# Kernel optimization log

Hardware: AMD Instinct MI355X
Metric: run time of the kernel (lower is better)

## Reference

```python
import jax, jax.numpy as jnp
import numpy as np

N_NODES = 20000
N_EDGES = 320000
F_IN = 128
H = 4        # heads per layer
D = 128      # per-head hidden dim
NEG_SLOPE = 0.2


def setup_inputs() -> dict:
    key = jax.random.key(0)
    ks = jax.random.split(key, 14)
    s = 0.05
    inp = {
        "feats": jax.random.normal(ks[0], (N_NODES, F_IN), jnp.float32),
        "src": jax.random.randint(ks[1], (N_EDGES,), 0, N_NODES, jnp.int64),
        "dst": jax.random.randint(ks[2], (N_EDGES,), 0, N_NODES, jnp.int64),
        # layer 1: in F_IN -> H heads x D, flatten agg
        "W1": s * jax.random.normal(ks[3], (F_IN, H * D), jnp.float32),
        "al1": s * jax.random.normal(ks[4], (H, D), jnp.float32),
        "ar1": s * jax.random.normal(ks[5], (H, D), jnp.float32),
        "b1": jnp.zeros((H * D,), jnp.float32),
        # layer 2: in H*D -> H heads x D, mean agg
        "W2": s * jax.random.normal(ks[6], (H * D, H * D), jnp.float32),
        "al2": s * jax.random.normal(ks[7], (H, D), jnp.float32),
        "ar2": s * jax.random.normal(ks[8], (H, D), jnp.float32),
        "b2": jnp.zeros((H * D,), jnp.float32),
        # readout Linear(D, 1)
        "Wr": s * jax.random.normal(ks[9], (D, 1), jnp.float32),
        "br": jnp.zeros((1,), jnp.float32),
    }
    return inp


def _gat_conv(x, src, dst, W, al, ar, b, n_nodes):
    """dgl GATConv: per-head linear, edge softmax over incoming edges, scatter-sum."""
    h, d = al.shape
    z = (x @ W).reshape(n_nodes, h, d)                      # [N,H,D]
    el = jnp.einsum('nhd,hd->nh', z, al)                    # [N,H]
    er = jnp.einsum('nhd,hd->nh', z, ar)                    # [N,H]
    e = jax.nn.leaky_relu(el[src] + er[dst], NEG_SLOPE)     # [E,H]
    # numerically stable softmax grouped by destination node
    emax = jax.lax.stop_gradient(jax.ops.segment_max(e, dst, num_segments=n_nodes))
    a = jnp.exp(e - emax[dst])                              # [E,H]
    denom = jax.ops.segment_sum(a, dst, num_segments=n_nodes)
    alpha = a / jnp.maximum(denom[dst], 1e-9)               # [E,H]
    out = jax.ops.segment_sum(alpha[:, :, None] * z[src], dst, num_segments=n_nodes)
    return out + b.reshape(1, h, d)                         # [N,H,D]


def reference(feats, src, dst, W1, al1, ar1, b1, W2, al2, ar2, b2, Wr, br):
    n = feats.shape[0]
    h1 = _gat_conv(feats, src, dst, W1, al1, ar1, b1, n)    # [N,H,D]
    h1 = jax.nn.elu(h1.reshape(n, -1))                      # flatten heads -> [N,H*D]
    h2 = _gat_conv(h1, src, dst, W2, al2, ar2, b2, n)       # [N,H,D]
    h2 = h2.mean(axis=1)                                    # mean over heads -> [N,D]
    node_preds = h2 @ Wr + br                               # [N,1]
    return node_preds.sum(axis=0)                           # [1]
```

## Files before the change

### kernel.cpp

```cpp
#include <hip/hip_runtime.h>
#include <hip/hip_bf16.h>
#include <cstddef>

constexpr int NN = 20000;
constexpr int NE = 320000;
constexpr int NHEAD = 4;
constexpr int ND = 128;
constexpr int HD = 512;
constexpr int MPAD = 20096;
constexpr int SLOTS = 64;
constexpr float NEG_SLOPE = 0.2f;

using short8 = __attribute__((ext_vector_type(8))) short;
using f32x4 = __attribute__((ext_vector_type(4))) float;
using f32x2 = __attribute__((ext_vector_type(2))) float;

__device__ inline void gload16(const void* g, void* l) {
  __builtin_amdgcn_global_load_lds(
      (const __attribute__((address_space(1))) void*)g,
      (__attribute__((address_space(3))) void*)l, 16, 0, 0);
}

__device__ inline unsigned char f32_to_fp8(float v) {
  int pk = __builtin_amdgcn_cvt_pk_fp8_f32(v, v, 0, false);
  return (unsigned char)(pk & 0xff);
}

__global__ __launch_bounds__(256) void fill_kernel(const int* __restrict__ dst,
                                                   const int* __restrict__ src,
                                                   int* __restrict__ cnt,
                                                   int* __restrict__ src_perm) {
  int t = blockIdx.x * 256 + threadIdx.x;
  if (t < NE) {
    int d = dst[t];
    int p = atomicAdd(&cnt[d], 1);
    if (p < SLOTS) src_perm[d * SLOTS + p] = src[t];
  }
}

constexpr int P0 = MPAD * 128;
constexpr int P1 = P0 + 512 * 128;
constexpr int P2 = P1 + 512 * 512;
constexpr int P3 = P2 + (MPAD - NN) * HD;
constexpr int P4 = P3 + 256;
__global__ __launch_bounds__(256) void prep_kernel(
    const float* __restrict__ feats, const float* __restrict__ W1,
    const float* __restrict__ W2,
    __hip_bfloat16* __restrict__ featsb, __hip_bfloat16* __restrict__ W1t,
    __hip_bfloat16* __restrict__ W2t, __hip_bfloat16* __restrict__ hb,
    float* __restrict__ partials) {
  int t = blockIdx.x * 256 + threadIdx.x;
  if (t < P0) {
    featsb[t] = __float2bfloat16(t < NN * 128 ? feats[t] : 0.f);
  } else if (t < P1) {
    int u = t - P0;
    W1t[u] = __float2bfloat16(W1[(size_t)(u & 127) * 512 + (u >> 7)]);
  } else if (t < P2) {
    int u = t - P1;
    W2t[u] = __float2bfloat16(W2[(size_t)(u & 511) * 512 + (u >> 9)]);
  } else if (t < P3) {
    int u = t - P2;
    hb[(size_t)NN * HD + u] = __float2bfloat16(0.f);
  } else if (t < P4) {
    partials[t - P3] = 0.f;
  }
}

__global__ __launch_bounds__(256) void mfma_gemm_kernel(
    const __hip_bfloat16* __restrict__ A,
    const __hip_bfloat16* __restrict__ Bt,
    unsigned char* __restrict__ Cout,
    int K,
    const float* __restrict__ al,
    const float* __restrict__ ar,
    const float* __restrict__ wq,
    float* __restrict__ el,
    float* __restrict__ er,
    float* __restrict__ q) {
  __shared__ short As[128 * 32];
  __shared__ short Bs[128 * 32];
  __shared__ float elbuf[4][128];
  __shared__ float erbuf[4][128];
  __shared__ float qbuf[4][128];
  int t = threadIdx.x;
  int lane = t & 63;
  int wave = t >> 6;
  int rowBase = blockIdx.x * 128;
  int head = blockIdx.y;
  int colBase = head * 128;
  int woffr = (wave & 1) * 64;
  int woffc = (wave >> 1) * 64;
  int mrow = lane & 15, quad = lane >> 4;

  f32x4 acc[4][4];
#pragma unroll
  for (int i = 0; i < 4; ++i)
#pragma unroll
    for (int j = 0; j < 4; ++j) acc[i][j] = (f32x4){0.f, 0.f, 0.f, 0.f};

  for (int k0 = 0; k0 < K; k0 += 32) {
#pragma unroll
    for (int p = 0; p < 2; ++p) {
      int f = p * 256 + wave * 64 + lane;
      int r = f >> 2, kc = f & 3;
      gload16(A + (size_t)(rowBase + r) * K + k0 + kc * 8,
              As + p * 2048 + wave * 512);
      gload16(Bt + (size_t)(colBase + r) * K + k0 + kc * 8,
              Bs + p * 2048 + wave * 512);
    }
    __syncthreads();
    short8 af[4], bfr[4];
#pragma unroll
    for (int i = 0; i < 4; ++i)
      af[i] = *(const short8*)&As[(woffr + i * 16 + mrow) * 32 + quad * 8];
#pragma unroll
    for (int j = 0; j < 4; ++j)
      bfr[j] = *(const short8*)&Bs[(woffc + j * 16 + mrow) * 32 + quad * 8];
#pragma unroll
    for (int i = 0; i < 4; ++i)
#pragma unroll
      for (int j = 0; j < 4; ++j)
        acc[i][j] = __builtin_amdgcn_mfma_f32_16x16x32_bf16(af[i], bfr[j], acc[i][j], 0, 0, 0);
    __syncthreads();
  }

  if (Cout) {
#pragma unroll
    for (int i = 0; i < 4; ++i) {
#pragma unroll
      for (int j = 0; j < 4; ++j) {
        int col = colBase + woffc + j * 16 + mrow;
#pragma unroll
        for (int r = 0; r < 4; ++r) {
          int row = rowBase + woffr + i * 16 + quad * 4 + r;
          Cout[(size_t)row * HD + col] = f32_to_fp8(acc[i][j][r]);
        }
      }
    }
  }

  float al_v[4], ar_v[4], wq_v[4];
#pragma unroll
  for (int j = 0; j < 4; ++j) {
    int coll = woffc + j * 16 + mrow;
    al_v[j] = al[head * 128 + coll];
    ar_v[j] = ar[head * 128 + coll];
    wq_v[j] = wq ? wq[coll] : 0.f;
  }
#pragma unroll
  for (int i = 0; i < 4; ++i) {
#pragma unroll
    for (int r = 0; r < 4; ++r) {
      float pl = 0.f, pr = 0.f, pq = 0.f;
#pragma unroll
      for (int j = 0; j < 4; ++j) {
        float v = acc[i][j][r];
        pl += v * al_v[j];
        pr += v * ar_v[j];
        pq += v * wq_v[j];
      }
#pragma unroll
      for (int off = 1; off < 16; off <<= 1) {
        pl += __shfl_xor(pl, off);
        pr += __shfl_xor(pr, off);
        pq += __shfl_xor(pq, off);
      }
      if (mrow == 0) {
        int row128 = woffr + i * 16 + quad * 4 + r;
        elbuf[wave][row128] = pl;
        erbuf[wave][row128] = pr;
        qbuf[wave][row128] = pq;
      }
    }
  }
  __syncthreads();
  if (t < 128) {
    int row = t;
    int w0 = (row < 64) ? 0 : 1;
    float ev = elbuf[w0][row] + elbuf[w0 + 2][row];
    float rv = erbuf[w0][row] + erbuf[w0 + 2][row];
    float qv = qbuf[w0][row] + qbuf[w0 + 2][row];
    int gr = rowBase + row;
    if (gr < NN) {
      el[gr * 4 + head] = ev;
      er[gr * 4 + head] = rv;
      if (wq) q[gr * 4 + head] = qv;
    }
  }
}

__global__ __launch_bounds__(256) void aggregate_kernel(
    const unsigned char* __restrict__ zf8,
    const int* __restrict__ cnt,
    const int* __restrict__ src_perm,
    const float* __restrict__ el,
    const float* __restrict__ er,
    const float* __restrict__ bias,
    __hip_bfloat16* __restrict__ out) {
  __shared__ float4 alds[4][SLOTS];
  int wv = __builtin_amdgcn_readfirstlane((int)(threadIdx.x >> 6));
  int n = blockIdx.x * 4 + wv;
  int lane = threadIdx.x & 63;
  int c = min(cnt[n], SLOTS);
  int base = n * SLOTS;

  {
    float4 er4 = *reinterpret_cast<const float4*>(&er[n * 4]);
    float a0 = 0.f, a1 = 0.f, a2 = 0.f, a3 = 0.f;
    if (lane < c) {
      int s = src_perm[base + lane];
      float4 e4 = *reinterpret_cast<const float4*>(&el[s * 4]);
      float x0 = e4.x + er4.x, x1 = e4.y + er4.y;
      float x2 = e4.z + er4.z, x3 = e4.w + er4.w;
      x0 = (x0 > 0.f) ? x0 : NEG_SLOPE * x0;
      x1 = (x1 > 0.f) ? x1 : NEG_SLOPE * x1;
      x2 = (x2 > 0.f) ? x2 : NEG_SLOPE * x2;
      x3 = (x3 > 0.f) ? x3 : NEG_SLOPE * x3;
      a0 = __expf(x0); a1 = __expf(x1); a2 = __expf(x2); a3 = __expf(x3);
    }
    float s0 = a0, s1 = a1, s2 = a2, s3 = a3;
#pragma unroll
    for (int off = 1; off < 64; off <<= 1) {
      s0 += __shfl_xor(s0, off);
      s1 += __shfl_xor(s1, off);
      s2 += __shfl_xor(s2, off);
      s3 += __shfl_xor(s3, off);
    }
    float4 av;
    av.x = a0 / fmaxf(s0, 1e-9f);
    av.y = a1 / fmaxf(s1, 1e-9f);
    av.z = a2 / fmaxf(s2, 1e-9f);
    av.w = a3 / fmaxf(s3, 1e-9f);
    alds[wv][lane] = av;
  }

  int head = lane >> 4;
  float acc[8] = {};

#define EDGE_BODY(IDX)                                                         \
  {                                                                            \
    int s = src_perm[base + (IDX)];                                            \
    float4 a4 = alds[wv][(IDX)];                                               \
    float a = (head & 2) ? ((head & 1) ? a4.w : a4.z)                          \
                         : ((head & 1) ? a4.y : a4.x);                         \
    uint2 w = *reinterpret_cast<const uint2*>(zf8 + (size_t)s * 512 + lane * 8); \
    f32x2 f0 = __builtin_amdgcn_cvt_pk_f32_fp8(w.x, false);                    \
    f32x2 f1 = __builtin_amdgcn_cvt_pk_f32_fp8(w.x, true);                     \
    f32x2 f2 = __builtin_amdgcn_cvt_pk_f32_fp8(w.y, false);                    \
    f32x2 f3 = __builtin_amdgcn_cvt_pk_f32_fp8(w.y, true);                     \
    acc[0] += a * f0.x; acc[1] += a * f0.y;                                    \
    acc[2] += a * f1.x; acc[3] += a * f1.y;                                    \
    acc[4] += a * f2.x; acc[5] += a * f2.y;                                    \
    acc[6] += a * f3.x; acc[7] += a * f3.y;                                    \
  }

  int i = 0;
  for (; i + 3 < c; i += 4) {
    EDGE_BODY(i)
    EDGE_BODY(i + 1)
    EDGE_BODY(i + 2)
    EDGE_BODY(i + 3)
  }
  for (; i < c; ++i) EDGE_BODY(i)
#undef EDGE_BODY

  float4 bA = *reinterpret_cast<const float4*>(&bias[lane * 8]);
  float4 bB = *reinterpret_cast<const float4*>(&bias[lane * 8 + 4]);
  float v[8];
  v[0] = acc[0] + bA.x; v[1] = acc[1] + bA.y;
  v[2] = acc[2] + bA.z; v[3] = acc[3] + bA.w;
  v[4] = acc[4] + bB.x; v[5] = acc[5] + bB.y;
  v[6] = acc[6] + bB.z; v[7] = acc[7] + bB.w;
#pragma unroll
  for (int j = 0; j < 8; ++j) v[j] = (v[j] > 0.f) ? v[j] : expm1f(v[j]);
  __hip_bfloat162 o[4];
#pragma unroll
  for (int j = 0; j < 4; ++j)
    o[j] = __float22bfloat162_rn(make_float2(v[2 * j], v[2 * j + 1]));
  *reinterpret_cast<uint4*>(out + (size_t)n * HD + lane * 8) =
      *reinterpret_cast<const uint4*>(o);
}

__global__ __launch_bounds__(256) void attn_q_kernel(
    const int* __restrict__ src_perm,
    const int* __restrict__ cnt,
    const float* __restrict__ el,
    const float* __restrict__ er,
    const float* __restrict__ q,
    float* __restrict__ partials) {
  __shared__ float blk[4];
  int wv = __builtin_amdgcn_readfirstlane((int)(threadIdx.x >> 6));
  int n = blockIdx.x * 4 + wv;
  int lane = threadIdx.x & 63;
  int c = min(cnt[n], SLOTS);
  float4 er4 = *reinterpret_cast<const float4*>(&er[n * 4]);
  float a0 = 0.f, a1 = 0.f, a2 = 0.f, a3 = 0.f;
  int s = 0;
  if (lane < c) {
    s = src_perm[n * SLOTS + lane];
    float4 e4 = *reinterpret_cast<const float4*>(&el[s * 4]);
    float x0 = e4.x + er4.x, x1 = e4.y + er4.y;
    float x2 = e4.z + er4.z, x3 = e4.w + er4.w;
    x0 = (x0 > 0.f) ? x0 : NEG_SLOPE * x0;
    x1 = (x1 > 0.f) ? x1 : NEG_SLOPE * x1;
    x2 = (x2 > 0.f) ? x2 : NEG_SLOPE * x2;
    x3 = (x3 > 0.f) ? x3 : NEG_SLOPE * x3;
    a0 = __expf(x0); a1 = __expf(x1); a2 = __expf(x2); a3 = __expf(x3);
  }
  float s0 = a0, s1 = a1, s2 = a2, s3 = a3;
#pragma unroll
  for (int off = 1; off < 64; off <<= 1) {
    s0 += __shfl_xor(s0, off);
    s1 += __shfl_xor(s1, off);
    s2 += __shfl_xor(s2, off);
    s3 += __shfl_xor(s3, off);
  }
  float p = 0.f;
  if (lane < c) {
    float4 q4 = *reinterpret_cast<const float4*>(&q[s * 4]);
    p = (a0 / fmaxf(s0, 1e-9f)) * q4.x + (a1 / fmaxf(s1, 1e-9f)) * q4.y +
        (a2 / fmaxf(s2, 1e-9f)) * q4.z + (a3 / fmaxf(s3, 1e-9f)) * q4.w;
  }
#pragma unroll
  for (int off = 32; off > 0; off >>= 1) p += __shfl_down(p, off);
  if (lane == 0) blk[wv] = p;
  __syncthreads();
  if (threadIdx.x == 0) {
    atomicAdd(&partials[blockIdx.x & 255], blk[0] + blk[1] + blk[2] + blk[3]);
  }
}

__global__ __launch_bounds__(512) void final_kernel(
    const float* __restrict__ partials, const float* __restrict__ b2,
    const float* __restrict__ Wr, const float* __restrict__ br,
    float* __restrict__ out) {
  __shared__ float tmp[512];
  int t = threadIdx.x;
  float sum = (t < 256) ? partials[t] : 0.f;
  sum += (float)NN * b2[t] * Wr[t & 127];
  tmp[t] = sum;
  __syncthreads();
  for (int off = 256; off > 0; off >>= 1) {
    if (t < off) tmp[t] += tmp[t + off];
    __syncthreads();
  }
  if (t == 0) out[0] = 0.25f * tmp[0] + (float)NN * br[0];
}

extern "C" void kernel_launch(void* const* d_in, const int* in_sizes, int n_in,
                              void* d_out, int out_size, void* d_ws, size_t ws_size,
                              hipStream_t stream) {
  const float* feats = (const float*)d_in[0];
  const int* src = (const int*)d_in[1];
  const int* dst = (const int*)d_in[2];
  const float* W1 = (const float*)d_in[3];
  const float* al1 = (const float*)d_in[4];
  const float* ar1 = (const float*)d_in[5];
  const float* b1 = (const float*)d_in[6];
  const float* W2 = (const float*)d_in[7];
  const float* al2 = (const float*)d_in[8];
  const float* ar2 = (const float*)d_in[9];
  const float* b2 = (const float*)d_in[10];
  const float* Wr = (const float*)d_in[11];
  const float* br = (const float*)d_in[12];
  float* out = (float*)d_out;

  __hip_bfloat16* featsb = (__hip_bfloat16*)d_ws;
  unsigned char* zf8 = (unsigned char*)(featsb + (size_t)MPAD * 128);
  __hip_bfloat16* hb = (__hip_bfloat16*)(zf8 + (size_t)MPAD * HD);
  __hip_bfloat16* W1t = hb + (size_t)MPAD * HD;
  __hip_bfloat16* W2t = W1t + 512 * 128;
  float* el = (float*)(W2t + 512 * 512);
  float* er = el + (size_t)NN * NHEAD;
  float* qv = er + (size_t)NN * NHEAD;
  float* partials = qv + (size_t)NN * NHEAD;
  int* cnt = (int*)(partials + 256);
  int* src_perm = cnt + NN;

  hipMemsetAsync(cnt, 0, NN * sizeof(int), stream);
  fill_kernel<<<(NE + 255) / 256, 256, 0, stream>>>(dst, src, cnt, src_perm);

  prep_kernel<<<(P4 + 255) / 256, 256, 0, stream>>>(feats, W1, W2, featsb, W1t,
                                                    W2t, hb, partials);

  dim3 gemm_grid(MPAD / 128, NHEAD);

  mfma_gemm_kernel<<<gemm_grid, 256, 0, stream>>>(featsb, W1t, zf8, 128,
                                                  al1, ar1, nullptr, el, er, nullptr);
  aggregate_kernel<<<NN / 4, 256, 0, stream>>>(zf8, cnt, src_perm, el, er, b1, hb);

  mfma_gemm_kernel<<<gemm_grid, 256, 0, stream>>>(hb, W2t, nullptr, 512,
                                                  al2, ar2, Wr, el, er, qv);
  attn_q_kernel<<<NN / 4, 256, 0, stream>>>(src_perm, cnt, el, er, qv, partials);
  final_kernel<<<1, 512, 0, stream>>>(partials, b2, Wr, br, out);
}
```

Measured before the change: 193.7 us.

## Fold layer-2 GEMM into precomputed projection vectors fused into aggregation

Layer 2 only needs el2, er2 and the readout projection q per node and head. So W2 is pre-multiplied with al2, ar2 and Wr into 12 combined 512-length vectors. The aggregation kernel then dots each ELU output row with these vectors directly. This removes the second 20000x512x512 MFMA GEMM, the bf16 h1 buffer write and the W2 transpose. It also merges fill into prep and folds the final reduction into attn_q through a last-block atomic counter, which drops two launches. The cost is extra per-wave shuffle reductions in aggregate and a serial 128-long dot per thread in prep.

```diff
diff --git a/kernel.cpp b/kernel.cpp
--- a/kernel.cpp
+++ b/kernel.cpp
@@ -26,62 +26,60 @@
   return (unsigned char)(pk & 0xff);
 }
 
-__global__ __launch_bounds__(256) void fill_kernel(const int* __restrict__ dst,
-                                                   const int* __restrict__ src,
-                                                   int* __restrict__ cnt,
-                                                   int* __restrict__ src_perm) {
+constexpr int S0 = NE;
+constexpr int S1 = S0 + MPAD * 128;
+constexpr int S2 = S1 + 512 * 128;
+constexpr int S3 = S2 + 12 * 512;
+constexpr int S4 = S3 + 256;
+constexpr int S5 = S4 + 16;
+__global__ __launch_bounds__(256) void prep_kernel(
+    const float* __restrict__ feats, const float* __restrict__ W1,
+    const float* __restrict__ W2, const float* __restrict__ al2,
+    const float* __restrict__ ar2, const float* __restrict__ Wr,
+    const int* __restrict__ src, const int* __restrict__ dst,
+    __hip_bfloat16* __restrict__ featsb, __hip_bfloat16* __restrict__ W1t,
+    float* __restrict__ vcomb, float* __restrict__ partials,
+    unsigned int* __restrict__ done,
+    int* __restrict__ cnt, int* __restrict__ src_perm) {
   int t = blockIdx.x * 256 + threadIdx.x;
-  if (t < NE) {
+  if (t < S0) {
     int d = dst[t];
     int p = atomicAdd(&cnt[d], 1);
     if (p < SLOTS) src_perm[d * SLOTS + p] = src[t];
-  }
-}
-
-constexpr int P0 = MPAD * 128;
-constexpr int P1 = P0 + 512 * 128;
-constexpr int P2 = P1 + 512 * 512;
-constexpr int P3 = P2 + (MPAD - NN) * HD;
-constexpr int P4 = P3 + 256;
-__global__ __launch_bounds__(256) void prep_kernel(
-    const float* __restrict__ feats, const float* __restrict__ W1,
-    const float* __restrict__ W2,
-    __hip_bfloat16* __restrict__ featsb, __hip_bfloat16* __restrict__ W1t,
-    __hip_bfloat16* __restrict__ W2t, __hip_bfloat16* __restrict__ hb,
-    float* __restrict__ partials) {
-  int t = blockIdx.x * 256 + threadIdx.x;
-  if (t < P0) {
-    featsb[t] = __float2bfloat16(t < NN * 128 ? feats[t] : 0.f);
-  } else if (t < P1) {
-    int u = t - P0;
+  } else if (t < S1) {
+    int u = t - S0;
+    featsb[u] = __float2bfloat16(u < NN * 128 ? feats[u] : 0.f);
+  } else if (t < S2) {
+    int u = t - S1;
     W1t[u] = __float2bfloat16(W1[(size_t)(u & 127) * 512 + (u >> 7)]);
-  } else if (t < P2) {
-    int u = t - P1;
-    W2t[u] = __float2bfloat16(W2[(size_t)(u & 511) * 512 + (u >> 9)]);
-  } else if (t < P3) {
-    int u = t - P2;
-    hb[(size_t)NN * HD + u] = __float2bfloat16(0.f);
-  } else if (t < P4) {
-    partials[t - P3] = 0.f;
-  }
-}
-
-__global__ __launch_bounds__(256) void mfma_gemm_kernel(
+  } else if (t < S3) {
+    int u = t - S2;
+    int v = u >> 9, k = u & 511;
+    int h = (v < 4) ? v : (v < 8) ? v - 4 : v - 8;
+    const float* vec = (v < 4) ? (al2 + h * 128)
+                     : (v < 8) ? (ar2 + h * 128) : Wr;
+    const float* wrow = W2 + (size_t)k * 512 + h * 128;
+    float s = 0.f;
+    for (int d = 0; d < 128; ++d) s += wrow[d] * vec[d];
+    vcomb[u] = s;
+  } else if (t < S4) {
+    partials[t - S3] = 0.f;
+  } else if (t < S5) {
+    if (t == S4) *done = 0u;
+  }
+}
+
+__global__ __launch_bounds__(256) void gemm1_kernel(
     const __hip_bfloat16* __restrict__ A,
     const __hip_bfloat16* __restrict__ Bt,
-    unsigned char* __restrict__ Cout,
-    int K,
-    const float* __restrict__ al,
-    const float* __restrict__ ar,
-    const float* __restrict__ wq,
-    float* __restrict__ el,
-    float* __restrict__ er,
-    float* __restrict__ q) {
+    unsigned char* __restrict__ C,
+    const float* __restrict__ al, const float* __restrict__ ar,
+    float* __restrict__ el, float* __restrict__ er) {
+  constexpr int K = 128;
   __shared__ short As[128 * 32];
   __shared__ short Bs[128 * 32];
   __shared__ float elbuf[4][128];
   __shared__ float erbuf[4][128];
-  __shared__ float qbuf[4][128];
   int t = threadIdx.x;
   int lane = t & 63;
   int wave = t >> 6;
@@ -124,52 +122,46 @@
     __syncthreads();
   }
 
-  if (Cout) {
-#pragma unroll
-    for (int i = 0; i < 4; ++i) {
-#pragma unroll
-      for (int j = 0; j < 4; ++j) {
-        int col = colBase + woffc + j * 16 + mrow;
-#pragma unroll
-        for (int r = 0; r < 4; ++r) {
-          int row = rowBase + woffr + i * 16 + quad * 4 + r;
-          Cout[(size_t)row * HD + col] = f32_to_fp8(acc[i][j][r]);
-        }
+#pragma unroll
+  for (int i = 0; i < 4; ++i) {
+#pragma unroll
+    for (int j = 0; j < 4; ++j) {
+      int col = colBase + woffc + j * 16 + mrow;
+#pragma unroll
+      for (int r = 0; r < 4; ++r) {
+        int row = rowBase + woffr + i * 16 + quad * 4 + r;
+        C[(size_t)row * HD + col] = f32_to_fp8(acc[i][j][r]);
       }
     }
   }
 
-  float al_v[4], ar_v[4], wq_v[4];
+  float al_v[4], ar_v[4];
 #pragma unroll
   for (int j = 0; j < 4; ++j) {
     int coll = woffc + j * 16 + mrow;
     al_v[j] = al[head * 128 + coll];
     ar_v[j] = ar[head * 128 + coll];
-    wq_v[j] = wq ? wq[coll] : 0.f;
   }
 #pragma unroll
   for (int i = 0; i < 4; ++i) {
 #pragma unroll
     for (int r = 0; r < 4; ++r) {
-      float pl = 0.f, pr = 0.f, pq = 0.f;
+      float pl = 0.f, pr = 0.f;
 #pragma unroll
       for (int j = 0; j < 4; ++j) {
         float v = acc[i][j][r];
         pl += v * al_v[j];
         pr += v * ar_v[j];
-        pq += v * wq_v[j];
       }
 #pragma unroll
       for (int off = 1; off < 16; off <<= 1) {
         pl += __shfl_xor(pl, off);
         pr += __shfl_xor(pr, off);
-        pq += __shfl_xor(pq, off);
       }
       if (mrow == 0) {
         int row128 = woffr + i * 16 + quad * 4 + r;
         elbuf[wave][row128] = pl;
         erbuf[wave][row128] = pr;
-        qbuf[wave][row128] = pq;
       }
     }
   }
@@ -179,12 +171,10 @@
     int w0 = (row < 64) ? 0 : 1;
     float ev = elbuf[w0][row] + elbuf[w0 + 2][row];
     float rv = erbuf[w0][row] + erbuf[w0 + 2][row];
-    float qv = qbuf[w0][row] + qbuf[w0 + 2][row];
     int gr = rowBase + row;
     if (gr < NN) {
       el[gr * 4 + head] = ev;
       er[gr * 4 + head] = rv;
-      if (wq) q[gr * 4 + head] = qv;
     }
   }
 }
@@ -195,8 +185,11 @@
     const int* __restrict__ src_perm,
     const float* __restrict__ el,
     const float* __restrict__ er,
-    const float* __restrict__ bias,
-    __hip_bfloat16* __restrict__ out) {
+    const float* __restrict__ b1,
+    const float* __restrict__ vcomb,
+    float* __restrict__ el2,
+    float* __restrict__ er2,
+    float* __restrict__ q2) {
   __shared__ float4 alds[4][SLOTS];
   int wv = __builtin_amdgcn_readfirstlane((int)(threadIdx.x >> 6));
   int n = blockIdx.x * 4 + wv;
@@ -264,8 +257,8 @@
   for (; i < c; ++i) EDGE_BODY(i)
 #undef EDGE_BODY
 
-  float4 bA = *reinterpret_cast<const float4*>(&bias[lane * 8]);
-  float4 bB = *reinterpret_cast<const float4*>(&bias[lane * 8 + 4]);
+  float4 bA = *reinterpret_cast<const float4*>(&b1[lane * 8]);
+  float4 bB = *reinterpret_cast<const float4*>(&b1[lane * 8 + 4]);
   float v[8];
   v[0] = acc[0] + bA.x; v[1] = acc[1] + bA.y;
   v[2] = acc[2] + bA.z; v[3] = acc[3] + bA.w;
@@ -273,12 +266,24 @@
   v[6] = acc[6] + bB.z; v[7] = acc[7] + bB.w;
 #pragma unroll
   for (int j = 0; j < 8; ++j) v[j] = (v[j] > 0.f) ? v[j] : expm1f(v[j]);
-  __hip_bfloat162 o[4];
-#pragma unroll
-  for (int j = 0; j < 4; ++j)
-    o[j] = __float22bfloat162_rn(make_float2(v[2 * j], v[2 * j + 1]));
-  *reinterpret_cast<uint4*>(out + (size_t)n * HD + lane * 8) =
-      *reinterpret_cast<const uint4*>(o);
+
+  float r[12];
+#pragma unroll
+  for (int vv = 0; vv < 12; ++vv) {
+    const float* vb = vcomb + vv * 512 + lane * 8;
+    float4 cA = *reinterpret_cast<const float4*>(vb);
+    float4 cB = *reinterpret_cast<const float4*>(vb + 4);
+    float p = v[0] * cA.x + v[1] * cA.y + v[2] * cA.z + v[3] * cA.w +
+              v[4] * cB.x + v[5] * cB.y + v[6] * cB.z + v[7] * cB.w;
+#pragma unroll
+    for (int off = 1; off < 64; off <<= 1) p += __shfl_xor(p, off);
+    r[vv] = p;
+  }
+  if (lane == 0) {
+    *reinterpret_cast<float4*>(&el2[n * 4]) = make_float4(r[0], r[1], r[2], r[3]);
+    *reinterpret_cast<float4*>(&er2[n * 4]) = make_float4(r[4], r[5], r[6], r[7]);
+    *reinterpret_cast<float4*>(&q2[n * 4]) = make_float4(r[8], r[9], r[10], r[11]);
+  }
 }
 
 __global__ __launch_bounds__(256) void attn_q_kernel(
@@ -287,8 +292,13 @@
     const float* __restrict__ el,
     const float* __restrict__ er,
     const float* __restrict__ q,
-    float* __restrict__ partials) {
+    float* __restrict__ partials,
+    unsigned int* __restrict__ done,
+    const float* __restrict__ b2, const float* __restrict__ Wr,
+    const float* __restrict__ br, float* __restrict__ out) {
   __shared__ float blk[4];
+  __shared__ float tmp[256];
+  __shared__ int lastflag;
   int wv = __builtin_amdgcn_readfirstlane((int)(threadIdx.x >> 6));
   int n = blockIdx.x * 4 + wv;
   int lane = threadIdx.x & 63;
@@ -327,24 +337,23 @@
   __syncthreads();
   if (threadIdx.x == 0) {
     atomicAdd(&partials[blockIdx.x & 255], blk[0] + blk[1] + blk[2] + blk[3]);
-  }
-}
-
-__global__ __launch_bounds__(512) void final_kernel(
-    const float* __restrict__ partials, const float* __restrict__ b2,
-    const float* __restrict__ Wr, const float* __restrict__ br,
-    float* __restrict__ out) {
-  __shared__ float tmp[512];
-  int t = threadIdx.x;
-  float sum = (t < 256) ? partials[t] : 0.f;
-  sum += (float)NN * b2[t] * Wr[t & 127];
-  tmp[t] = sum;
+    __threadfence();
+    unsigned prev = atomicAdd(done, 1u);
+    lastflag = (prev == gridDim.x - 1) ? 1 : 0;
+  }
   __syncthreads();
-  for (int off = 256; off > 0; off >>= 1) {
-    if (t < off) tmp[t] += tmp[t + off];
+  if (lastflag) {
+    int t = threadIdx.x;
+    float sum = atomicAdd(&partials[t], 0.0f);
+    sum += (float)NN * (b2[t] + b2[t + 256]) * Wr[t & 127];
+    tmp[t] = sum;
     __syncthreads();
-  }
-  if (t == 0) out[0] = 0.25f * tmp[0] + (float)NN * br[0];
+    for (int off = 128; off > 0; off >>= 1) {
+      if (t < off) tmp[t] += tmp[t + off];
+      __syncthreads();
+    }
+    if (t == 0) out[0] = 0.25f * tmp[0] + (float)NN * br[0];
+  }
 }
 
 extern "C" void kernel_launch(void* const* d_in, const int* in_sizes, int n_in,
@@ -367,30 +376,30 @@
 
   __hip_bfloat16* featsb = (__hip_bfloat16*)d_ws;
   unsigned char* zf8 = (unsigned char*)(featsb + (size_t)MPAD * 128);
-  __hip_bfloat16* hb = (__hip_bfloat16*)(zf8 + (size_t)MPAD * HD);
-  __hip_bfloat16* W1t = hb + (size_t)MPAD * HD;
-  __hip_bfloat16* W2t = W1t + 512 * 128;
-  float* el = (float*)(W2t + 512 * 512);
-  float* er = el + (size_t)NN * NHEAD;
-  float* qv = er + (size_t)NN * NHEAD;
-  float* partials = qv + (size_t)NN * NHEAD;
-  int* cnt = (int*)(partials + 256);
+  __hip_bfloat16* W1t = (__hip_bfloat16*)(zf8 + (size_t)MPAD * HD);
+  float* vcomb = (float*)(W1t + 512 * 128);
+  float* el1 = vcomb + 12 * 512;
+  float* er1 = el1 + (size_t)NN * NHEAD;
+  float* el2 = er1 + (size_t)NN * NHEAD;
+  float* er2 = el2 + (size_t)NN * NHEAD;
+  float* q2 = er2 + (size_t)NN * NHEAD;
+  float* partials = q2 + (size_t)NN * NHEAD;
+  unsigned int* done = (unsigned int*)(partials + 256);
+  int* cnt = (int*)(done + 4);
   int* src_perm = cnt + NN;
 
   hipMemsetAsync(cnt, 0, NN * sizeof(int), stream);
-  fill_kernel<<<(NE + 255) / 256, 256, 0, stream>>>(dst, src, cnt, src_perm);
-
-  prep_kernel<<<(P4 + 255) / 256, 256, 0, stream>>>(feats, W1, W2, featsb, W1t,
-                                                    W2t, hb, partials);
+  prep_kernel<<<(S5 + 255) / 256, 256, 0, stream>>>(
+      feats, W1, W2, al2, ar2, Wr, src, dst, featsb, W1t, vcomb, partials,
+      done, cnt, src_perm);
 
   dim3 gemm_grid(MPAD / 128, NHEAD);
 
-  mfma_gemm_kernel<<<gemm_grid, 256, 0, stream>>>(featsb, W1t, zf8, 128,
-                                                  al1, ar1, nullptr, el, er, nullptr);
-  aggregate_kernel<<<NN / 4, 256, 0, stream>>>(zf8, cnt, src_perm, el, er, b1, hb);
-
-  mfma_gemm_kernel<<<gemm_grid, 256, 0, stream>>>(hb, W2t, nullptr, 512,
-                                                  al2, ar2, Wr, el, er, qv);
-  attn_q_kernel<<<NN / 4, 256, 0, stream>>>(src_perm, cnt, el, er, qv, partials);
-  final_kernel<<<1, 512, 0, stream>>>(partials, b2, Wr, br, out);
-}
+  gemm1_kernel<<<gemm_grid, 256, 0, stream>>>(featsb, W1t, zf8, al1, ar1, el1, er1);
+
+  aggregate_kernel<<<NN / 4, 256, 0, stream>>>(zf8, cnt, src_perm, el1, er1, b1,
+                                               vcomb, el2, er2, q2);
+
+  attn_q_kernel<<<NN / 4, 256, 0, stream>>>(src_perm, cnt, el2, er2, q2,
+                                            partials, done, b2, Wr, br, out);
+}
```

After: 259.3 us. 1.34x slower.
